# Kernel tuning notes

Measured on AMD Instinct MI355X. Metric: run time of the kernel, lower is better.

The kernel has to match this reference:

```python
import jax, jax.numpy as jnp
import numpy as np

B, S, DIM, N, D = 1, 3072, 2048, 16, 128
EPS = 1e-06


def rms_norm(x, w, eps=EPS):
    # x: [B, S, C]; normalize over last dim (matches npu_rms_norm)
    var = jnp.mean(jnp.square(x), axis=-1, keepdims=True)
    return x * jax.lax.rsqrt(var + eps) * w


def rope_interleave(x, cos, sin):
    # x: [B, S, N, D]; cos/sin: [B, S, 1, D] with pairwise-repeated values.
    # interleave mode: (x0, x1) -> (x0*c - x1*s, x1*c + x0*s) for adjacent pairs.
    xe = x[..., 0::2]
    xo = x[..., 1::2]
    rot = jnp.stack([-xo, xe], axis=-1).reshape(x.shape)
    return (x * cos + rot * sin).astype(jnp.float32)  # rope_apply casts to float


def setup_inputs() -> dict:
    key = jax.random.key(0)
    ks = jax.random.split(key, 16)
    sd = 1.0 / np.sqrt(DIM)
    inp = {
        'x': jax.random.normal(ks[0], (B, S, DIM), jnp.float32),
        'Wq': jax.random.normal(ks[1], (DIM, DIM), jnp.float32) * sd,
        'bq': jax.random.normal(ks[2], (DIM,), jnp.float32) * 0.01,
        'Wk': jax.random.normal(ks[3], (DIM, DIM), jnp.float32) * sd,
        'bk': jax.random.normal(ks[4], (DIM,), jnp.float32) * 0.01,
        'Wv': jax.random.normal(ks[5], (DIM, DIM), jnp.float32) * sd,
        'bv': jax.random.normal(ks[6], (DIM,), jnp.float32) * 0.01,
        'Wo': jax.random.normal(ks[7], (DIM, DIM), jnp.float32) * sd,
        'bo': jax.random.normal(ks[8], (DIM,), jnp.float32) * 0.01,
        'norm_q_w': jnp.ones((DIM,), jnp.float32),
        'norm_k_w': jnp.ones((DIM,), jnp.float32),
    }
    # per-sample 3D rope folded into precomputed interleaved cos/sin tables
    pos = jnp.arange(S, dtype=jnp.float32)
    inv = 1.0 / (10000.0 ** (jnp.arange(D // 2, dtype=jnp.float32) / (D // 2)))
    ang = pos[:, None] * inv[None, :]                    # [S, D/2]
    cos = jnp.repeat(jnp.cos(ang), 2, axis=-1)           # [S, D] pairwise repeated
    sin = jnp.repeat(jnp.sin(ang), 2, axis=-1)
    inp['rope_cos'] = jnp.broadcast_to(cos[None, :, None, :], (B, S, 1, D))
    inp['rope_sin'] = jnp.broadcast_to(sin[None, :, None, :], (B, S, 1, D))
    inp['seq_lens'] = jax.random.randint(ks[9], (B,), S // 2, S + 1).astype(jnp.int32)
    inp['grid_sizes'] = jnp.broadcast_to(jnp.array([[12, 16, 16]], jnp.int32), (B, 3))
    return inp


def reference(x, Wq, bq, Wk, bk, Wv, bv, Wo, bo, norm_q_w, norm_k_w,
              rope_cos, rope_sin, seq_lens, grid_sizes):
    b, s, _ = x.shape
    # fused QKV projection + RMSNorm on q/k
    q = rms_norm(x @ Wq.T + bq, norm_q_w).reshape(b, s, N, D)
    k = rms_norm(x @ Wk.T + bk, norm_k_w).reshape(b, s, N, D)
    v = (x @ Wv.T + bv).reshape(b, s, N, D)
    # per-sample interleaved RoPE (outputs float32, as in rope_apply)
    q = rope_interleave(q, rope_cos, rope_sin)
    k = rope_interleave(k, rope_cos, rope_sin)
    # full attention with key-length masking (window_size = (-1, -1))
    scale = 1.0 / np.sqrt(D)
    scores = jnp.einsum('bqnd,bknd->bnqk', q, k) * scale    # [B, N, S, S]
    kmask = jnp.arange(s)[None, :] < seq_lens[:, None]       # [B, S]
    scores = jnp.where(kmask[:, None, None, :], scores, jnp.float32(-1e30))
    probs = jax.nn.softmax(scores, axis=-1)
    out = jnp.einsum('bnqk,bknd->bqnd', probs, v.astype(jnp.float32))
    out = out.reshape(b, s, N * D)
    return out @ Wo.T + bo
```

## Files before the change

kernel.cpp:

```cpp
#include <hip/hip_runtime.h>

typedef __attribute__((ext_vector_type(8))) short short8;
typedef __attribute__((ext_vector_type(4))) float f32x4;

#define SQ 3072
#define DM 2048
#define NHEAD 16
#define HDIM 128

__device__ __forceinline__ unsigned short f2bf(float f) {
  union { float f; unsigned int u; } un; un.f = f;
  unsigned int r = un.u + 0x7fffu + ((un.u >> 16) & 1u);
  return (unsigned short)(r >> 16);
}

__device__ __forceinline__ void gload_lds16(const void* g, void* l) {
  __builtin_amdgcn_global_load_lds(
      (const __attribute__((address_space(1))) void*)g,
      (__attribute__((address_space(3))) void*)l, 16, 0, 0);
}

__global__ __launch_bounds__(256) void cvt_bf16(const float* __restrict__ in,
                                                unsigned short* __restrict__ out, int n) {
  int i = (blockIdx.x * 256 + threadIdx.x) * 8;
  if (i >= n) return;
  float4 a = *(const float4*)(in + i);
  float4 b = *(const float4*)(in + i + 4);
  short8 r;
  r[0] = (short)f2bf(a.x); r[1] = (short)f2bf(a.y);
  r[2] = (short)f2bf(a.z); r[3] = (short)f2bf(a.w);
  r[4] = (short)f2bf(b.x); r[5] = (short)f2bf(b.y);
  r[6] = (short)f2bf(b.z); r[7] = (short)f2bf(b.w);
  *(short8*)(out + i) = r;
}

__global__ __launch_bounds__(256) void gemm_nt_bias(
    const unsigned short* __restrict__ A, const unsigned short* __restrict__ B,
    const float* __restrict__ b0, const float* __restrict__ b1, const float* __restrict__ b2,
    float* __restrict__ C, int M, int N, int K)
{
  __shared__ __align__(16) unsigned short As[128 * 64];
  __shared__ __align__(16) unsigned short Bs[128 * 64];
  const int tid = threadIdx.x;
  const int wave = tid >> 6, lane = tid & 63;
  const int wm = wave >> 1, wn = wave & 1;
  const int m0 = blockIdx.y * 128, n0 = blockIdx.x * 128;
  const int lr = lane & 15, lg = lane >> 4;
  const int srow = lane >> 3, scol = (lane & 7) * 8;
  f32x4 acc[4][4] = {};
  for (int k0 = 0; k0 < K; k0 += 64) {
    #pragma unroll
    for (int i = 0; i < 4; ++i) {
      int rg = i * 4 + wave;
      int r = rg * 8 + srow;
      gload_lds16(A + (size_t)(m0 + r) * K + k0 + scol, &As[rg * 512]);
      gload_lds16(B + (size_t)(n0 + r) * K + k0 + scol, &Bs[rg * 512]);
    }
    __syncthreads();
    #pragma unroll
    for (int kk = 0; kk < 2; ++kk) {
      short8 af[4], bfr[4];
      #pragma unroll
      for (int m = 0; m < 4; ++m)
        af[m] = *(const short8*)&As[(wm * 64 + m * 16 + lr) * 64 + kk * 32 + lg * 8];
      #pragma unroll
      for (int n = 0; n < 4; ++n)
        bfr[n] = *(const short8*)&Bs[(wn * 64 + n * 16 + lr) * 64 + kk * 32 + lg * 8];
      #pragma unroll
      for (int m = 0; m < 4; ++m) {
        #pragma unroll
        for (int n = 0; n < 4; ++n)
          acc[m][n] = __builtin_amdgcn_mfma_f32_16x16x32_bf16(af[m], bfr[n], acc[m][n], 0, 0, 0);
      }
    }
    __syncthreads();
  }
  const float* bp = (n0 < DM) ? b0 : ((n0 < 2 * DM) ? b1 : b2);
  #pragma unroll
  for (int n = 0; n < 4; ++n) {
    int col = n0 + wn * 64 + n * 16 + lr;
    float bv = bp[col & (DM - 1)];
    #pragma unroll
    for (int m = 0; m < 4; ++m) {
      int row = m0 + wm * 64 + m * 16 + lg * 4;
      #pragma unroll
      for (int j = 0; j < 4; ++j)
        C[(size_t)(row + j) * N + col] = acc[m][n][j] + bv;
    }
  }
}

__global__ __launch_bounds__(256) void normrope(
    const float* __restrict__ qkv, const float* __restrict__ nqw, const float* __restrict__ nkw,
    const float* __restrict__ cosb, const float* __restrict__ sinb,
    unsigned short* __restrict__ Qb, unsigned short* __restrict__ Kb)
{
  const int s = blockIdx.x, z = blockIdx.y;
  const float* row = qkv + ((size_t)s * 3 + z) * DM;
  const float* gw = z ? nkw : nqw;
  unsigned short* ob = z ? Kb : Qb;
  const int t = threadIdx.x;
  float v[8];
  {
    float4 a = *(const float4*)(row + t * 8);
    float4 b = *(const float4*)(row + t * 8 + 4);
    v[0] = a.x; v[1] = a.y; v[2] = a.z; v[3] = a.w;
    v[4] = b.x; v[5] = b.y; v[6] = b.z; v[7] = b.w;
  }
  float ss = 0.f;
  #pragma unroll
  for (int i = 0; i < 8; ++i) ss += v[i] * v[i];
  #pragma unroll
  for (int off = 1; off < 64; off <<= 1) ss += __shfl_xor(ss, off);
  __shared__ float red[4];
  const int wave = t >> 6, lane = t & 63;
  if (lane == 0) red[wave] = ss;
  __syncthreads();
  float tot = red[0] + red[1] + red[2] + red[3];
  float rsc = rsqrtf(tot * (1.0f / 2048.0f) + 1e-6f);
  const float qs = z ? 1.0f : 0.12751879522087045f;
  const int col = t * 8, d = col & 127, h = col >> 7;
  const float* cb = cosb + (size_t)s * HDIM + d;
  const float* sb = sinb + (size_t)s * HDIM + d;
  float y[8];
  #pragma unroll
  for (int i = 0; i < 8; ++i) y[i] = v[i] * rsc * gw[col + i];
  short8 r;
  #pragma unroll
  for (int p = 0; p < 4; ++p) {
    float e = y[2 * p], o = y[2 * p + 1];
    float c0 = cb[2 * p], s0 = sb[2 * p];
    float c1 = cb[2 * p + 1], s1 = sb[2 * p + 1];
    r[2 * p]     = (short)f2bf((e * c0 - o * s0) * qs);
    r[2 * p + 1] = (short)f2bf((o * c1 + e * s1) * qs);
  }
  *(short8*)(ob + ((size_t)h * SQ + s) * HDIM + d) = r;
}

__global__ __launch_bounds__(256) void vtrans(const float* __restrict__ V, int ldv,
                                              unsigned short* __restrict__ Vt)
{
  __shared__ float tile[64][65];
  const int db = blockIdx.x * 64, sb = blockIdx.y * 64, h = blockIdx.z;
  const int t = threadIdx.x;
  const int rr = t >> 2, c0 = (t & 3) * 16;
  const float* src = V + (size_t)(sb + rr) * ldv + h * HDIM + db + c0;
  #pragma unroll
  for (int i = 0; i < 4; ++i) {
    float4 a = *(const float4*)(src + i * 4);
    tile[rr][c0 + i * 4 + 0] = a.x; tile[rr][c0 + i * 4 + 1] = a.y;
    tile[rr][c0 + i * 4 + 2] = a.z; tile[rr][c0 + i * 4 + 3] = a.w;
  }
  __syncthreads();
  const int dr = t >> 2, s0 = (t & 3) * 16;
  short8 r0, r1;
  #pragma unroll
  for (int i = 0; i < 8; ++i) r0[i] = (short)f2bf(tile[s0 + i][dr]);
  #pragma unroll
  for (int i = 0; i < 8; ++i) r1[i] = (short)f2bf(tile[s0 + 8 + i][dr]);
  unsigned short* dst = Vt + ((size_t)h * HDIM + db + dr) * SQ + sb + s0;
  *(short8*)(dst) = r0;
  *(short8*)(dst + 8) = r1;
}

__global__ __launch_bounds__(256) void attn(
    const unsigned short* __restrict__ Qb, const unsigned short* __restrict__ Kb,
    const unsigned short* __restrict__ Vt, const int* __restrict__ seq_lens,
    unsigned short* __restrict__ aout)
{
  __shared__ __align__(16) unsigned short Ks[64 * 136];
  __shared__ __align__(16) unsigned short Vs[128 * 72];
  __shared__ __align__(16) unsigned short Ps[4][16 * 72];
  const int tid = threadIdx.x, wave = tid >> 6, lane = tid & 63;
  const int h = blockIdx.y, q0 = blockIdx.x * 64;
  const int lr = lane & 15, lg = lane >> 4;
  const int seq_len = seq_lens[0];

  short8 qf[4];
  {
    const unsigned short* qrow = Qb + ((size_t)h * SQ + q0 + wave * 16 + lr) * HDIM;
    #pragma unroll
    for (int kk = 0; kk < 4; ++kk)
      qf[kk] = *(const short8*)(qrow + kk * 32 + lg * 8);
  }
  f32x4 o[8] = {};
  float lsum[4] = {0.f, 0.f, 0.f, 0.f};

  for (int kt = 0; kt < seq_len; kt += 64) {
    #pragma unroll
    for (int c = 0; c < 4; ++c) {
      int lin = c * 256 + tid;
      int krow = lin >> 4, kc = (lin & 15) * 8;
      short8 tv = *(const short8*)(Kb + ((size_t)h * SQ + kt + krow) * HDIM + kc);
      *(short8*)&Ks[krow * 136 + kc] = tv;
    }
    #pragma unroll
    for (int c = 0; c < 4; ++c) {
      int lin = c * 256 + tid;
      int vrow = lin >> 3, vc = (lin & 7) * 8;
      short8 tv = *(const short8*)(Vt + ((size_t)h * HDIM + vrow) * SQ + kt + vc);
      *(short8*)&Vs[vrow * 72 + vc] = tv;
    }
    __syncthreads();

    f32x4 sf[4] = {};
    #pragma unroll
    for (int kk = 0; kk < 4; ++kk) {
      #pragma unroll
      for (int n = 0; n < 4; ++n) {
        short8 kf = *(const short8*)&Ks[(n * 16 + lr) * 136 + kk * 32 + lg * 8];
        sf[n] = __builtin_amdgcn_mfma_f32_16x16x32_bf16(qf[kk], kf, sf[n], 0, 0, 0);
      }
    }
    if (kt + 64 > seq_len) {
      #pragma unroll
      for (int n = 0; n < 4; ++n) {
        if (kt + n * 16 + lr >= seq_len) {
          #pragma unroll
          for (int j = 0; j < 4; ++j) sf[n][j] = -3.0e38f;
        }
      }
    }
    unsigned short* Pw = &Ps[wave][0];
    #pragma unroll
    for (int n = 0; n < 4; ++n) {
      #pragma unroll
      for (int j = 0; j < 4; ++j) {
        float p = exp2f(sf[n][j]);
        lsum[j] += p;
        Pw[(lg * 4 + j) * 72 + n * 16 + lr] = f2bf(p);
      }
    }
    #pragma unroll
    for (int kk = 0; kk < 2; ++kk) {
      short8 pa = *(const short8*)&Pw[lr * 72 + kk * 32 + lg * 8];
      #pragma unroll
      for (int dn = 0; dn < 8; ++dn) {
        short8 vb = *(const short8*)&Vs[(dn * 16 + lr) * 72 + kk * 32 + lg * 8];
        o[dn] = __builtin_amdgcn_mfma_f32_16x16x32_bf16(pa, vb, o[dn], 0, 0, 0);
      }
    }
    __syncthreads();
  }
  #pragma unroll
  for (int off = 1; off < 16; off <<= 1) {
    #pragma unroll
    for (int j = 0; j < 4; ++j) lsum[j] += __shfl_xor(lsum[j], off);
  }
  float rcp[4];
  #pragma unroll
  for (int j = 0; j < 4; ++j) rcp[j] = 1.0f / lsum[j];
  #pragma unroll
  for (int dn = 0; dn < 8; ++dn) {
    int col = h * HDIM + dn * 16 + lr;
    #pragma unroll
    for (int j = 0; j < 4; ++j) {
      int row = q0 + wave * 16 + lg * 4 + j;
      aout[(size_t)row * DM + col] = f2bf(o[dn][j] * rcp[j]);
    }
  }
}

extern "C" void kernel_launch(void* const* d_in, const int* in_sizes, int n_in,
                              void* d_out, int out_size, void* d_ws, size_t ws_size,
                              hipStream_t stream) {
  const float* x   = (const float*)d_in[0];
  const float* Wq  = (const float*)d_in[1];
  const float* bq  = (const float*)d_in[2];
  const float* Wk  = (const float*)d_in[3];
  const float* bk  = (const float*)d_in[4];
  const float* Wv  = (const float*)d_in[5];
  const float* bv  = (const float*)d_in[6];
  const float* Wo  = (const float*)d_in[7];
  const float* bo  = (const float*)d_in[8];
  const float* nqw = (const float*)d_in[9];
  const float* nkw = (const float*)d_in[10];
  const float* rc  = (const float*)d_in[11];
  const float* rs  = (const float*)d_in[12];
  const int* seql  = (const int*)d_in[13];
  float* out = (float*)d_out;

  unsigned short* xb   = (unsigned short*)d_ws;
  unsigned short* Wqkv = xb   + (size_t)SQ * DM;
  unsigned short* Wob  = Wqkv + (size_t)3 * DM * DM;
  float* qkv           = (float*)(Wob + (size_t)DM * DM);
  unsigned short* Qb   = (unsigned short*)(qkv + (size_t)3 * SQ * DM);
  unsigned short* Kb   = Qb + (size_t)SQ * DM;
  unsigned short* Vt   = Kb + (size_t)SQ * DM;
  unsigned short* aob  = Vt + (size_t)SQ * DM;

  const int nx = SQ * DM, nw = DM * DM;
  cvt_bf16<<<nx / 2048, 256, 0, stream>>>(x, xb, nx);
  cvt_bf16<<<nw / 2048, 256, 0, stream>>>(Wq, Wqkv, nw);
  cvt_bf16<<<nw / 2048, 256, 0, stream>>>(Wk, Wqkv + (size_t)nw, nw);
  cvt_bf16<<<nw / 2048, 256, 0, stream>>>(Wv, Wqkv + (size_t)2 * nw, nw);
  cvt_bf16<<<nw / 2048, 256, 0, stream>>>(Wo, Wob, nw);

  dim3 gq(3 * DM / 128, SQ / 128);
  gemm_nt_bias<<<gq, 256, 0, stream>>>(xb, Wqkv, bq, bk, bv, qkv, SQ, 3 * DM, DM);

  normrope<<<dim3(SQ, 2), 256, 0, stream>>>(qkv, nqw, nkw, rc, rs, Qb, Kb);
  vtrans<<<dim3(2, SQ / 64, NHEAD), 256, 0, stream>>>(qkv + 2 * DM, 3 * DM, Vt);

  attn<<<dim3(SQ / 64, NHEAD), 256, 0, stream>>>(Qb, Kb, Vt, seql, aob);

  dim3 go(DM / 128, SQ / 128);
  gemm_nt_bias<<<go, 256, 0, stream>>>(aob, Wob, bo, bo, bo, out, SQ, DM, DM);
}
```

Baseline: 467.7 us.

## Triple-buffer GEMM LDS loads with swizzle and merge conversion kernels

The GEMM now uses a three-stage LDS ring buffer. Global-to-LDS loads are issued two tiles ahead and waited on with explicit vmcnt/barrier, so memory latency overlaps with MFMA work. LDS columns are XOR-swizzled to avoid bank conflicts, and MFMA sections are wrapped in s_setprio. The five fp32-to-bf16 conversion launches become one kernel. In exchange, LDS use rises to 96KB per block, which may lower occupancy.

```diff
diff --git a/kernel.cpp b/kernel.cpp
--- a/kernel.cpp
+++ b/kernel.cpp
@@ -20,18 +20,29 @@
       (__attribute__((address_space(3))) void*)l, 16, 0, 0);
 }
 
-__global__ __launch_bounds__(256) void cvt_bf16(const float* __restrict__ in,
-                                                unsigned short* __restrict__ out, int n) {
-  int i = (blockIdx.x * 256 + threadIdx.x) * 8;
-  if (i >= n) return;
-  float4 a = *(const float4*)(in + i);
-  float4 b = *(const float4*)(in + i + 4);
+__global__ __launch_bounds__(256) void cvt_all(
+    const float* __restrict__ x, const float* __restrict__ wq, const float* __restrict__ wk,
+    const float* __restrict__ wv, const float* __restrict__ wo,
+    unsigned short* __restrict__ xb, unsigned short* __restrict__ wqkvb,
+    unsigned short* __restrict__ wob)
+{
+  int b = blockIdx.x;
+  const float* src; unsigned short* dst; int idx;
+  if (b < 3072) { src = x; dst = xb; idx = b; }
+  else {
+    int r = b - 3072; int w = r >> 11; idx = r & 2047;
+    src = (w == 0) ? wq : (w == 1) ? wk : (w == 2) ? wv : wo;
+    dst = (w < 3) ? wqkvb + (size_t)w * DM * DM : wob;
+  }
+  int i = (idx * 256 + threadIdx.x) * 8;
+  float4 a = *(const float4*)(src + i);
+  float4 c = *(const float4*)(src + i + 4);
   short8 r;
   r[0] = (short)f2bf(a.x); r[1] = (short)f2bf(a.y);
   r[2] = (short)f2bf(a.z); r[3] = (short)f2bf(a.w);
-  r[4] = (short)f2bf(b.x); r[5] = (short)f2bf(b.y);
-  r[6] = (short)f2bf(b.z); r[7] = (short)f2bf(b.w);
-  *(short8*)(out + i) = r;
+  r[4] = (short)f2bf(c.x); r[5] = (short)f2bf(c.y);
+  r[6] = (short)f2bf(c.z); r[7] = (short)f2bf(c.w);
+  *(short8*)(dst + i) = r;
 }
 
 __global__ __launch_bounds__(256) void gemm_nt_bias(
@@ -39,42 +50,68 @@
     const float* __restrict__ b0, const float* __restrict__ b1, const float* __restrict__ b2,
     float* __restrict__ C, int M, int N, int K)
 {
-  __shared__ __align__(16) unsigned short As[128 * 64];
-  __shared__ __align__(16) unsigned short Bs[128 * 64];
+  __shared__ __align__(16) unsigned short lds[3 * 16384];
   const int tid = threadIdx.x;
   const int wave = tid >> 6, lane = tid & 63;
   const int wm = wave >> 1, wn = wave & 1;
   const int m0 = blockIdx.y * 128, n0 = blockIdx.x * 128;
   const int lr = lane & 15, lg = lane >> 4;
-  const int srow = lane >> 3, scol = (lane & 7) * 8;
+
+  const int srow = tid >> 3;
+  const int ks = (tid & 7) ^ (srow & 7);
+  const unsigned short* aSrc = A + (size_t)(m0 + srow) * K + ks * 8;
+  const unsigned short* bSrc = B + (size_t)(n0 + srow) * K + ks * 8;
+  const int dstOff = (tid & 192) * 8;
+
+  auto stage = [&](int t, int b) {
+    const unsigned short* as = aSrc + (size_t)t * 64;
+    const unsigned short* bs = bSrc + (size_t)t * 64;
+    unsigned short* la = &lds[b * 16384 + dstOff];
+    #pragma unroll
+    for (int c = 0; c < 4; ++c) {
+      gload_lds16(as + (size_t)c * 32 * K, la + c * 2048);
+      gload_lds16(bs + (size_t)c * 32 * K, la + 8192 + c * 2048);
+    }
+  };
+
   f32x4 acc[4][4] = {};
-  for (int k0 = 0; k0 < K; k0 += 64) {
-    #pragma unroll
-    for (int i = 0; i < 4; ++i) {
-      int rg = i * 4 + wave;
-      int r = rg * 8 + srow;
-      gload_lds16(A + (size_t)(m0 + r) * K + k0 + scol, &As[rg * 512]);
-      gload_lds16(B + (size_t)(n0 + r) * K + k0 + scol, &Bs[rg * 512]);
-    }
-    __syncthreads();
+  const int nt = K >> 6;
+  stage(0, 0);
+  stage(1, 1);
+  asm volatile("s_waitcnt vmcnt(8)\n\ts_barrier" ::: "memory");
+
+  const int sx = lr & 7;
+  const int arow = wm * 64 + lr;
+  const int brow = wn * 64 + lr;
+  for (int t = 0; t < nt; ++t) {
+    const unsigned short* La = &lds[(t % 3) * 16384];
+    const unsigned short* Lb = La + 8192;
+    if (t + 2 < nt) stage(t + 2, (t + 2) % 3);
+    short8 af[2][4], bfr[2][4];
     #pragma unroll
     for (int kk = 0; kk < 2; ++kk) {
-      short8 af[4], bfr[4];
       #pragma unroll
       for (int m = 0; m < 4; ++m)
-        af[m] = *(const short8*)&As[(wm * 64 + m * 16 + lr) * 64 + kk * 32 + lg * 8];
+        af[kk][m] = *(const short8*)&La[(arow + m * 16) * 64 + (((kk * 4 + lg) ^ sx) << 3)];
       #pragma unroll
       for (int n = 0; n < 4; ++n)
-        bfr[n] = *(const short8*)&Bs[(wn * 64 + n * 16 + lr) * 64 + kk * 32 + lg * 8];
+        bfr[kk][n] = *(const short8*)&Lb[(brow + n * 16) * 64 + (((kk * 4 + lg) ^ sx) << 3)];
+    }
+    __builtin_amdgcn_s_setprio(1);
+    #pragma unroll
+    for (int kk = 0; kk < 2; ++kk) {
       #pragma unroll
       for (int m = 0; m < 4; ++m) {
         #pragma unroll
         for (int n = 0; n < 4; ++n)
-          acc[m][n] = __builtin_amdgcn_mfma_f32_16x16x32_bf16(af[m], bfr[n], acc[m][n], 0, 0, 0);
-      }
-    }
-    __syncthreads();
-  }
+          acc[m][n] = __builtin_amdgcn_mfma_f32_16x16x32_bf16(af[kk][m], bfr[kk][n], acc[m][n], 0, 0, 0);
+      }
+    }
+    __builtin_amdgcn_s_setprio(0);
+    if (t + 2 < nt) asm volatile("s_waitcnt vmcnt(8)\n\ts_barrier" ::: "memory");
+    else            asm volatile("s_waitcnt vmcnt(0)\n\ts_barrier" ::: "memory");
+  }
+
   const float* bp = (n0 < DM) ? b0 : ((n0 < 2 * DM) ? b1 : b2);
   #pragma unroll
   for (int n = 0; n < 4; ++n) {
@@ -289,12 +326,7 @@
   unsigned short* Vt   = Kb + (size_t)SQ * DM;
   unsigned short* aob  = Vt + (size_t)SQ * DM;
 
-  const int nx = SQ * DM, nw = DM * DM;
-  cvt_bf16<<<nx / 2048, 256, 0, stream>>>(x, xb, nx);
-  cvt_bf16<<<nw / 2048, 256, 0, stream>>>(Wq, Wqkv, nw);
-  cvt_bf16<<<nw / 2048, 256, 0, stream>>>(Wk, Wqkv + (size_t)nw, nw);
-  cvt_bf16<<<nw / 2048, 256, 0, stream>>>(Wv, Wqkv + (size_t)2 * nw, nw);
-  cvt_bf16<<<nw / 2048, 256, 0, stream>>>(Wo, Wob, nw);
+  cvt_all<<<3072 + 4 * 2048, 256, 0, stream>>>(x, Wq, Wk, Wv, Wo, xb, Wqkv, Wob);
 
   dim3 gq(3 * DM / 128, SQ / 128);
   gemm_nt_bias<<<gq, 256, 0, stream>>>(xb, Wqkv, bq, bk, bv, qkv, SQ, 3 * DM, DM);
```

After: 429.8 us. -8.1%, faster.
